# Kernel optimization log

Hardware: AMD Instinct MI355X
Metric: run time of the kernel (lower is better)

Reference implementation:

```python
import jax, jax.numpy as jnp
import numpy as np

B = 8192      # number of molecules (graphs)
T = 524288    # total flat candidates (avg 64 per graph, jagged)
D = 128       # embed_dim
V = 100000    # unique templates (table has V+1 rows incl. 'unknown')


def setup_inputs() -> dict:
    key = jax.random.key(0)
    k1, k2, k3 = jax.random.split(key, 3)
    rng = np.random.default_rng(0)
    # jagged lengths, each segment >= 1, summing exactly to T
    lengths = rng.multinomial(T - B, np.ones(B) / B) + 1
    seg_ids = np.repeat(np.arange(B), lengths)           # [T], sorted segment ids
    offsets = np.concatenate([[0], np.cumsum(lengths)[:-1]])
    target_pos = offsets + rng.integers(0, lengths)      # one target per segment
    return {
        "graph_embed": jax.random.normal(k1, (B, D), dtype=jnp.float32),
        "tpl_embedding": jax.random.normal(k2, (V + 1, D), dtype=jnp.float32),
        "cand_idx": jax.random.randint(k3, (T,), 0, V + 1),
        "seg_ids": jnp.asarray(seg_ids, dtype=jnp.int32),
        "target_pos": jnp.asarray(target_pos, dtype=jnp.int32),
    }


def reference(graph_embed, tpl_embedding, cand_idx, seg_ids, target_pos):
    num_seg = graph_embed.shape[0]
    # gather candidate (template) embeddings: [T, D]
    cand_embed = tpl_embedding[cand_idx]
    # gather graph embedding per candidate (torch.gather with rep_indices): [T, D]
    g = graph_embed[seg_ids]
    # inner-product attention score per candidate: [T]
    logits = jnp.sum(g * cand_embed, axis=1)
    # jagged (segment-wise) log-softmax over variable-length candidate lists
    seg_max = jax.ops.segment_max(logits, seg_ids, num_segments=num_seg)
    shifted = logits - seg_max[seg_ids]
    seg_sum = jax.ops.segment_sum(jnp.exp(shifted), seg_ids, num_segments=num_seg)
    log_prob = shifted - jnp.log(seg_sum)[seg_ids]
    # gather the log-prob of the target template per graph: [B]
    return log_prob[target_pos]
```

## Files before the change

kernel.cpp:

```cpp
#include <hip/hip_runtime.h>
#include <hip/hip_fp16.h>

#define D 128
#define LOG2E 1.4426950408889634f
#define LN2   0.6931471805599453f

__global__ __launch_bounds__(256) void tpl_half_kernel(
    const float4* __restrict__ src,
    uint2* __restrict__ dst,
    int n4)
{
    const int stride = gridDim.x * blockDim.x;
    for (int i = blockIdx.x * blockDim.x + threadIdx.x; i < n4; i += stride) {
        const float4 v = src[i];
        const __half2 h01 = __float22half2_rn(make_float2(v.x, v.y));
        const __half2 h23 = __float22half2_rn(make_float2(v.z, v.w));
        uint2 o;
        o.x = *reinterpret_cast<const unsigned*>(&h01);
        o.y = *reinterpret_cast<const unsigned*>(&h23);
        dst[i] = o;
    }
}

__global__ void seg_bounds_kernel(const int* __restrict__ seg_ids,
                                  int* __restrict__ seg_start,
                                  int T, int B) {
    int t = blockIdx.x * blockDim.x + threadIdx.x;
    if (t >= T) return;
    if (t == 0) seg_start[0] = 0;
    else if (seg_ids[t] != seg_ids[t - 1]) seg_start[seg_ids[t]] = t;
    if (t == T - 1) seg_start[B] = T;
}

__global__ __launch_bounds__(256) void logits_half_kernel(
    const float* __restrict__ graph_embed,
    const __half* __restrict__ tpl_h,
    const int* __restrict__ cand_idx,
    const int* __restrict__ seg_ids,
    float* __restrict__ logits,
    int T)
{
    const int sl  = threadIdx.x & 31;
    const int hw  = (blockIdx.x * blockDim.x + threadIdx.x) >> 5;
    const int nhw = (gridDim.x * blockDim.x) >> 5;

    for (int t0 = hw; t0 < T; t0 += 4 * nhw) {
        int  t[4];
        bool vld[4];
        #pragma unroll
        for (int j = 0; j < 4; ++j) {
            const int tj = t0 + j * nhw;
            vld[j] = (tj < T);
            t[j]   = vld[j] ? tj : t0;
        }

        int c[4], s[4];
        #pragma unroll
        for (int j = 0; j < 4; ++j) { c[j] = cand_idx[t[j]]; s[j] = seg_ids[t[j]]; }

        uint2  x[4];
        float4 g[4];
        #pragma unroll
        for (int j = 0; j < 4; ++j)
            x[j] = ((const uint2*)(tpl_h + (size_t)c[j] * D))[sl];
        #pragma unroll
        for (int j = 0; j < 4; ++j)
            g[j] = ((const float4*)(graph_embed + (size_t)s[j] * D))[sl];

        float p[4];
        #pragma unroll
        for (int j = 0; j < 4; ++j) {
            const float2 f01 = __half22float2(*reinterpret_cast<const __half2*>(&x[j].x));
            const float2 f23 = __half22float2(*reinterpret_cast<const __half2*>(&x[j].y));
            p[j] = fmaf(g[j].x, f01.x,
                   fmaf(g[j].y, f01.y,
                   fmaf(g[j].z, f23.x, g[j].w * f23.y)));
        }

        #pragma unroll
        for (int off = 16; off >= 1; off >>= 1) {
            #pragma unroll
            for (int j = 0; j < 4; ++j)
                p[j] += __shfl_xor(p[j], off);
        }

        if (sl == 0) {
            #pragma unroll
            for (int j = 0; j < 4; ++j)
                if (vld[j]) logits[t[j]] = p[j];
        }
    }
}

__global__ __launch_bounds__(256) void logits_kernel(
    const float* __restrict__ graph_embed,
    const float* __restrict__ tpl_embedding,
    const int* __restrict__ cand_idx,
    const int* __restrict__ seg_ids,
    float* __restrict__ logits,
    int T)
{
    const int sl  = threadIdx.x & 31;
    const int hw  = (blockIdx.x * blockDim.x + threadIdx.x) >> 5;
    const int nhw = (gridDim.x * blockDim.x) >> 5;

    for (int t0 = hw; t0 < T; t0 += 2 * nhw) {
        const int t1 = t0 + nhw;
        const bool has1 = (t1 < T);
        const int c0 = cand_idx[t0];
        const int s0 = seg_ids[t0];
        const int c1 = has1 ? cand_idx[t1] : c0;
        const int s1 = has1 ? seg_ids[t1] : s0;

        const float4 x0 = ((const float4*)(tpl_embedding + (size_t)c0 * D))[sl];
        const float4 g0 = ((const float4*)(graph_embed   + (size_t)s0 * D))[sl];
        const float4 x1 = ((const float4*)(tpl_embedding + (size_t)c1 * D))[sl];
        const float4 g1 = ((const float4*)(graph_embed   + (size_t)s1 * D))[sl];

        float p0 = fmaf(g0.x, x0.x, fmaf(g0.y, x0.y, fmaf(g0.z, x0.z, g0.w * x0.w)));
        float p1 = fmaf(g1.x, x1.x, fmaf(g1.y, x1.y, fmaf(g1.z, x1.z, g1.w * x1.w)));

        #pragma unroll
        for (int off = 16; off >= 1; off >>= 1) {
            p0 += __shfl_xor(p0, off);
            p1 += __shfl_xor(p1, off);
        }
        if (sl == 0) {
            logits[t0] = p0;
            if (has1) logits[t1] = p1;
        }
    }
}

__global__ __launch_bounds__(64) void seg_reduce_kernel(
    const float* __restrict__ logits,
    const int* __restrict__ seg_start,
    const int* __restrict__ target_pos,
    float* __restrict__ out)
{
    const int b    = blockIdx.x;
    const int lane = threadIdx.x;
    const int start = seg_start[b];
    const int end   = seg_start[b + 1];

    float m = -3.0e38f;
    float s = 0.0f;

    for (int t = start + lane; t < end; t += 64) {
        const float x = logits[t] * LOG2E;
        if (x <= m) {
            s += exp2f(x - m);
        } else {
            s = fmaf(s, exp2f(m - x), 1.0f);
            m = x;
        }
    }

    #pragma unroll
    for (int off = 32; off >= 1; off >>= 1) {
        const float m2 = __shfl_xor(m, off);
        const float s2 = __shfl_xor(s, off);
        const float M  = fmaxf(m, m2);
        s = s * exp2f(m - M) + s2 * exp2f(m2 - M);
        m = M;
    }

    if (lane == 0) {
        const float tl = logits[target_pos[b]] * LOG2E;
        out[b] = (tl - m - log2f(s)) * LN2;
    }
}

extern "C" void kernel_launch(void* const* d_in, const int* in_sizes, int n_in,
                              void* d_out, int out_size, void* d_ws, size_t ws_size,
                              hipStream_t stream) {
    const float* graph_embed   = (const float*)d_in[0];
    const float* tpl_embedding = (const float*)d_in[1];
    const int*   cand_idx      = (const int*)d_in[2];
    const int*   seg_ids       = (const int*)d_in[3];
    const int*   target_pos    = (const int*)d_in[4];
    float*       out           = (float*)d_out;

    const int B  = in_sizes[0] / D;
    const int VE = in_sizes[1];
    const int T  = in_sizes[2];

    size_t off = 0;
    auto alloc = [&](size_t bytes) {
        void* p = (char*)d_ws + off;
        off += (bytes + 255) & ~(size_t)255;
        return p;
    };
    int*    seg_start = (int*)   alloc((size_t)(B + 1) * 4);
    float*  logits    = (float*) alloc((size_t)T * 4);
    __half* tpl_h     = (__half*)alloc((size_t)VE * 2);

    seg_bounds_kernel<<<(T + 255) / 256, 256, 0, stream>>>(seg_ids, seg_start, T, B);

    if (off <= ws_size) {
        tpl_half_kernel<<<2048, 256, 0, stream>>>((const float4*)tpl_embedding,
                                                  (uint2*)tpl_h, VE / 4);
        logits_half_kernel<<<2048, 256, 0, stream>>>(graph_embed, tpl_h,
                                                     cand_idx, seg_ids, logits, T);
    } else {
        logits_kernel<<<2048, 256, 0, stream>>>(graph_embed, tpl_embedding,
                                                cand_idx, seg_ids, logits, T);
    }

    seg_reduce_kernel<<<B, 64, 0, stream>>>(logits, seg_start, target_pos, out);
}
```

Baseline: 133.3 us.

## Fuse prep kernels, convert graph embeddings to fp16, use fdot2 quarter-wave dot

Merges the template fp16 conversion and segment-bound detection into one prep kernel, which also converts graph embeddings to fp16. The logits kernel now uses 16 lanes per candidate with 16-byte loads and packed fp16 dot-product instructions, halving graph-row traffic and shortening the shuffle reduction. The aim is to cut one launch and reduce gather bandwidth and instruction count. In exchange, graph embeddings lose precision to fp16 and the dot products accumulate from fp16 products.

```diff
diff --git a/kernel.cpp b/kernel.cpp
--- a/kernel.cpp
+++ b/kernel.cpp
@@ -5,20 +5,99 @@
 #define LOG2E 1.4426950408889634f
 #define LN2   0.6931471805599453f
 
-__global__ __launch_bounds__(256) void tpl_half_kernel(
-    const float4* __restrict__ src,
-    uint2* __restrict__ dst,
-    int n4)
+__global__ __launch_bounds__(256) void prep_kernel(
+    const float4* __restrict__ tpl_src,
+    const float4* __restrict__ g_src,
+    uint2* __restrict__ tpl_dst,
+    uint2* __restrict__ g_dst,
+    const int* __restrict__ seg_ids,
+    int* __restrict__ seg_start,
+    int nt4, int ng4, int T, int B)
 {
     const int stride = gridDim.x * blockDim.x;
-    for (int i = blockIdx.x * blockDim.x + threadIdx.x; i < n4; i += stride) {
-        const float4 v = src[i];
+    const int tid0 = blockIdx.x * blockDim.x + threadIdx.x;
+
+    for (int i = tid0; i < nt4; i += stride) {
+        const float4 v = tpl_src[i];
         const __half2 h01 = __float22half2_rn(make_float2(v.x, v.y));
         const __half2 h23 = __float22half2_rn(make_float2(v.z, v.w));
         uint2 o;
         o.x = *reinterpret_cast<const unsigned*>(&h01);
         o.y = *reinterpret_cast<const unsigned*>(&h23);
-        dst[i] = o;
+        tpl_dst[i] = o;
+    }
+    for (int i = tid0; i < ng4; i += stride) {
+        const float4 v = g_src[i];
+        const __half2 h01 = __float22half2_rn(make_float2(v.x, v.y));
+        const __half2 h23 = __float22half2_rn(make_float2(v.z, v.w));
+        uint2 o;
+        o.x = *reinterpret_cast<const unsigned*>(&h01);
+        o.y = *reinterpret_cast<const unsigned*>(&h23);
+        g_dst[i] = o;
+    }
+    for (int t = tid0; t < T; t += stride) {
+        if (t == 0) seg_start[0] = 0;
+        else if (seg_ids[t] != seg_ids[t - 1]) seg_start[seg_ids[t]] = t;
+        if (t == T - 1) seg_start[B] = T;
+    }
+}
+
+__global__ __launch_bounds__(256) void logits_q_kernel(
+    const __half* __restrict__ graph_h,
+    const __half* __restrict__ tpl_h,
+    const int* __restrict__ cand_idx,
+    const int* __restrict__ seg_ids,
+    float* __restrict__ logits,
+    int T)
+{
+    const int sl  = threadIdx.x & 15;
+    const int qw  = (blockIdx.x * blockDim.x + threadIdx.x) >> 4;
+    const int nqw = (gridDim.x * blockDim.x) >> 4;
+
+    for (int t0 = qw; t0 < T; t0 += 2 * nqw) {
+        const int t1   = t0 + nqw;
+        const bool has1 = (t1 < T);
+        const int ta = t0, tb = has1 ? t1 : t0;
+
+        const int c0 = cand_idx[ta];
+        const int s0 = seg_ids[ta];
+        const int c1 = cand_idx[tb];
+        const int s1 = seg_ids[tb];
+
+        const uint4 x0 = ((const uint4*)(tpl_h   + (size_t)c0 * D))[sl];
+        const uint4 g0 = ((const uint4*)(graph_h + (size_t)s0 * D))[sl];
+        const uint4 x1 = ((const uint4*)(tpl_h   + (size_t)c1 * D))[sl];
+        const uint4 g1 = ((const uint4*)(graph_h + (size_t)s1 * D))[sl];
+
+        float p0 = 0.0f, p1 = 0.0f;
+        const __half2* xh0 = (const __half2*)&x0;
+        const __half2* gh0 = (const __half2*)&g0;
+        const __half2* xh1 = (const __half2*)&x1;
+        const __half2* gh1 = (const __half2*)&g1;
+        #pragma unroll
+        for (int k = 0; k < 4; ++k) {
+#if __has_builtin(__builtin_amdgcn_fdot2)
+            p0 = __builtin_amdgcn_fdot2(gh0[k], xh0[k], p0, false);
+            p1 = __builtin_amdgcn_fdot2(gh1[k], xh1[k], p1, false);
+#else
+            const float2 xf0 = __half22float2(xh0[k]);
+            const float2 gf0 = __half22float2(gh0[k]);
+            const float2 xf1 = __half22float2(xh1[k]);
+            const float2 gf1 = __half22float2(gh1[k]);
+            p0 = fmaf(gf0.x, xf0.x, fmaf(gf0.y, xf0.y, p0));
+            p1 = fmaf(gf1.x, xf1.x, fmaf(gf1.y, xf1.y, p1));
+#endif
+        }
+
+        #pragma unroll
+        for (int off = 8; off >= 1; off >>= 1) {
+            p0 += __shfl_xor(p0, off);
+            p1 += __shfl_xor(p1, off);
+        }
+        if (sl == 0) {
+            logits[ta] = p0;
+            if (has1) logits[tb] = p1;
+        }
     }
 }
 
@@ -30,66 +109,6 @@
     if (t == 0) seg_start[0] = 0;
     else if (seg_ids[t] != seg_ids[t - 1]) seg_start[seg_ids[t]] = t;
     if (t == T - 1) seg_start[B] = T;
-}
-
-__global__ __launch_bounds__(256) void logits_half_kernel(
-    const float* __restrict__ graph_embed,
-    const __half* __restrict__ tpl_h,
-    const int* __restrict__ cand_idx,
-    const int* __restrict__ seg_ids,
-    float* __restrict__ logits,
-    int T)
-{
-    const int sl  = threadIdx.x & 31;
-    const int hw  = (blockIdx.x * blockDim.x + threadIdx.x) >> 5;
-    const int nhw = (gridDim.x * blockDim.x) >> 5;
-
-    for (int t0 = hw; t0 < T; t0 += 4 * nhw) {
-        int  t[4];
-        bool vld[4];
-        #pragma unroll
-        for (int j = 0; j < 4; ++j) {
-            const int tj = t0 + j * nhw;
-            vld[j] = (tj < T);
-            t[j]   = vld[j] ? tj : t0;
-        }
-
-        int c[4], s[4];
-        #pragma unroll
-        for (int j = 0; j < 4; ++j) { c[j] = cand_idx[t[j]]; s[j] = seg_ids[t[j]]; }
-
-        uint2  x[4];
-        float4 g[4];
-        #pragma unroll
-        for (int j = 0; j < 4; ++j)
-            x[j] = ((const uint2*)(tpl_h + (size_t)c[j] * D))[sl];
-        #pragma unroll
-        for (int j = 0; j < 4; ++j)
-            g[j] = ((const float4*)(graph_embed + (size_t)s[j] * D))[sl];
-
-        float p[4];
-        #pragma unroll
-        for (int j = 0; j < 4; ++j) {
-            const float2 f01 = __half22float2(*reinterpret_cast<const __half2*>(&x[j].x));
-            const float2 f23 = __half22float2(*reinterpret_cast<const __half2*>(&x[j].y));
-            p[j] = fmaf(g[j].x, f01.x,
-                   fmaf(g[j].y, f01.y,
-                   fmaf(g[j].z, f23.x, g[j].w * f23.y)));
-        }
-
-        #pragma unroll
-        for (int off = 16; off >= 1; off >>= 1) {
-            #pragma unroll
-            for (int j = 0; j < 4; ++j)
-                p[j] += __shfl_xor(p[j], off);
-        }
-
-        if (sl == 0) {
-            #pragma unroll
-            for (int j = 0; j < 4; ++j)
-                if (vld[j]) logits[t[j]] = p[j];
-        }
-    }
 }
 
 __global__ __launch_bounds__(256) void logits_kernel(
@@ -181,7 +200,8 @@
     const int*   target_pos    = (const int*)d_in[4];
     float*       out           = (float*)d_out;
 
-    const int B  = in_sizes[0] / D;
+    const int BE = in_sizes[0];
+    const int B  = BE / D;
     const int VE = in_sizes[1];
     const int T  = in_sizes[2];
 
@@ -194,15 +214,18 @@
     int*    seg_start = (int*)   alloc((size_t)(B + 1) * 4);
     float*  logits    = (float*) alloc((size_t)T * 4);
     __half* tpl_h     = (__half*)alloc((size_t)VE * 2);
-
-    seg_bounds_kernel<<<(T + 255) / 256, 256, 0, stream>>>(seg_ids, seg_start, T, B);
+    __half* graph_h   = (__half*)alloc((size_t)BE * 2);
 
     if (off <= ws_size) {
-        tpl_half_kernel<<<2048, 256, 0, stream>>>((const float4*)tpl_embedding,
-                                                  (uint2*)tpl_h, VE / 4);
-        logits_half_kernel<<<2048, 256, 0, stream>>>(graph_embed, tpl_h,
-                                                     cand_idx, seg_ids, logits, T);
+        prep_kernel<<<2048, 256, 0, stream>>>((const float4*)tpl_embedding,
+                                              (const float4*)graph_embed,
+                                              (uint2*)tpl_h, (uint2*)graph_h,
+                                              seg_ids, seg_start,
+                                              VE / 4, BE / 4, T, B);
+        logits_q_kernel<<<2048, 256, 0, stream>>>(graph_h, tpl_h,
+                                                  cand_idx, seg_ids, logits, T);
     } else {
+        seg_bounds_kernel<<<(T + 255) / 256, 256, 0, stream>>>(seg_ids, seg_start, T, B);
         logits_kernel<<<2048, 256, 0, stream>>>(graph_embed, tpl_embedding,
                                                 cand_idx, seg_ids, logits, T);
     }
```

New measurement: 124.2 us. 6.8% less time.
